# Kernel optimization log

Hardware: AMD Instinct MI355X
Metric: run time of the kernel (lower is better)

Reference implementation:

```python
import jax, jax.numpy as jnp
import numpy as np
from jax import lax

NPOINT = 1024
NSAMPLE = 32
RADIUS = 0.2
EPS = 1e-5  # BatchNorm eps (torch default)


def farthest_point_sample(xyz, npoint):
    # xyz: [B, N, 3] -> [B, npoint] int32 indices. Deterministic start at index 0
    # (torch version uses a random start; math is otherwise identical).
    B, N, _ = xyz.shape

    def step(carry, _):
        distance, farthest = carry
        centroid = jnp.take_along_axis(xyz, farthest[:, None, None], axis=1)  # [B,1,3]
        d = jnp.sum((xyz - centroid) ** 2, axis=-1)                            # [B,N]
        distance = jnp.minimum(distance, d)
        return (distance, jnp.argmax(distance, axis=-1).astype(jnp.int32)), farthest

    init = (jnp.full((B, N), 1e10, xyz.dtype), jnp.zeros((B,), jnp.int32))
    _, cents = lax.scan(step, init, None, length=npoint)  # [npoint, B]
    return cents.T


def query_ball_point(radius, nsample, xyz, new_xyz):
    # xyz: [B,N,3], new_xyz: [B,S,3] -> [B,S,nsample] int32 indices
    B, N, _ = xyz.shape
    S = new_xyz.shape[1]
    sqr = jnp.sum((new_xyz[:, :, None, :] - xyz[:, None, :, :]) ** 2, axis=-1)  # [B,S,N]
    base = jnp.broadcast_to(jnp.arange(N, dtype=jnp.int32), (B, S, N))
    idx = jnp.where(sqr > radius * radius, N, base)
    idx = jnp.sort(idx, axis=-1)[:, :, :nsample]
    first = idx[:, :, :1]
    return jnp.where(idx == N, first, idx)


def index_points(points, idx):
    # points: [B,N,C], idx: [B,...] -> [B,...,C]
    return jax.vmap(lambda p, i: p[i])(points, idx)


def conv_bn_relu(x, w, b, g, beta):
    # 1x1 Conv2d == per-point linear; BatchNorm2d in training mode (batch stats,
    # biased variance) over all dims except channel.
    y = jnp.einsum('bskc,oc->bsko', x, w) + b          # [B,S,K,O]
    m = jnp.mean(y, axis=(0, 1, 2), keepdims=True)
    v = jnp.var(y, axis=(0, 1, 2), keepdims=True)
    return jax.nn.relu((y - m) / jnp.sqrt(v + EPS) * g + beta)


def setup_inputs() -> dict:
    key = jax.random.key(0)
    ks = jax.random.split(key, 8)
    B, N, D = 16, 4096, 64
    xyz = jax.random.uniform(ks[0], (B, N, 3), dtype=jnp.float32)
    points = jax.random.normal(ks[1], (B, N, D), dtype=jnp.float32)
    chans = [D + 3, 64, 64, 128]
    inp = {'xyz': xyz, 'points': points}
    for i in range(3):
        cin, cout = chans[i], chans[i + 1]
        inp[f'w{i}'] = jax.random.normal(ks[2 + i], (cout, cin), dtype=jnp.float32) * (1.0 / np.sqrt(cin))
        inp[f'b{i}'] = jnp.zeros((cout,), jnp.float32)
        inp[f'g{i}'] = jnp.ones((cout,), jnp.float32)
        inp[f'be{i}'] = jnp.zeros((cout,), jnp.float32)
    return inp


def reference(xyz, points, w0, b0, g0, be0, w1, b1, g1, be1, w2, b2, g2, be2):
    fps_idx = farthest_point_sample(xyz, NPOINT)            # [B,S]
    new_xyz = index_points(xyz, fps_idx)                    # [B,S,3]
    group_idx = query_ball_point(RADIUS, NSAMPLE, xyz, new_xyz)  # [B,S,K]
    grouped_xyz = index_points(xyz, group_idx) - new_xyz[:, :, None, :]  # [B,S,K,3]
    feats = jnp.concatenate([grouped_xyz, index_points(points, group_idx)], axis=-1)
    for (w, b, g, be) in ((w0, b0, g0, be0), (w1, b1, g1, be1), (w2, b2, g2, be2)):
        feats = conv_bn_relu(feats, w, b, g, be)
    new_points = jnp.max(feats, axis=2)                     # max over nsample -> [B,S,C_out]
    return new_xyz, new_points
```

## Files before the change

kernel.cpp:

```cpp
#include <hip/hip_runtime.h>
#include <hip/hip_bf16.h>
#include <cstdint>
#include <cstddef>

#define NPTS   4096
#define NPT    1024
#define NSAMP  32
#define NBATCH 16
#define MROWS  (NBATCH*NPT*NSAMP)
#define NTILES (MROWS / 64)
#define EPSV   1e-5f

typedef __attribute__((ext_vector_type(8))) short bfrag;
typedef __attribute__((ext_vector_type(4))) float f32x4;

static __device__ __forceinline__ unsigned short f2bf(float f) {
  union { float f; unsigned u; } x; x.f = f;
  unsigned u = x.u;
  u += 0x7FFFu + ((u >> 16) & 1u);
  return (unsigned short)(u >> 16);
}
static __device__ __forceinline__ float bf2f(unsigned short h) {
  union { unsigned u; float f; } x; x.u = ((unsigned)h) << 16;
  return x.f;
}
static __device__ __forceinline__ unsigned cvt_pk_bf16(float lo, float hi) {
  unsigned r;
  asm("v_cvt_pk_bf16_f32 %0, %1, %2" : "=v"(r) : "v"(lo), "v"(hi));
  return r;
}

__global__ __launch_bounds__(256) void prep_kernel(
    const float* __restrict__ w0, const float* __restrict__ w1,
    const float* __restrict__ w2, unsigned short* __restrict__ wb0,
    unsigned short* __restrict__ wb1, unsigned short* __restrict__ wb2,
    int* __restrict__ flags) {
  const int tid = threadIdx.x;
  for (int i = tid; i < 260; i += 256) flags[i] = 0;
  for (int i = tid; i < 64 * 96; i += 256) {
    const int o = i / 96, c = i % 96;
    float v;
    if (c < 64)      v = w0[o * 67 + 3 + c];
    else if (c < 67) v = w0[o * 67 + (c - 64)];
    else             v = 0.f;
    wb0[i] = f2bf(v);
  }
  for (int i = tid; i < 64 * 64; i += 256) wb1[i] = f2bf(w1[i]);
  for (int i = tid; i < 128 * 64; i += 256) wb2[i] = f2bf(w2[i]);
}

#define FPS_T 256
#define PPT   (NPTS / FPS_T)
#define CHUNK 128

template <int CTRL>
static __device__ __forceinline__ float dpp_max_step(float v) {
  int t = __builtin_amdgcn_update_dpp(0, __float_as_int(v), CTRL, 0xF, 0xF, true);
  return fmaxf(v, __int_as_float(t));
}

__global__ __launch_bounds__(256) void k1_kernel(
    const float* __restrict__ xyz, const float* __restrict__ points,
    const unsigned short* __restrict__ Wb, float* __restrict__ newxyz,
    unsigned short* __restrict__ Y1, float* __restrict__ psum,
    float* __restrict__ psq, int* __restrict__ flags) {
  __shared__ __align__(16) float xs[NPTS];
  __shared__ __align__(16) float ys[NPTS];
  __shared__ __align__(16) float zs[NPTS];
  __shared__ __align__(16) float olds[NPT * 3];
  __shared__ __align__(16) uint2 sl[2][4];
  constexpr int KP = 104;
  __shared__ __align__(16) unsigned short As[64 * KP];
  __shared__ __align__(16) unsigned short ly[64 * 64];
  __shared__ float ssum[64], ssq[64];
  __shared__ int   gidxL[64];
  __shared__ float cents[8];
  __shared__ int   s_tile;

  const int tid = threadIdx.x;
  int* progress = flags;
  int* counter  = flags + 256;

  if (blockIdx.x < NBATCH) {
    const int b = blockIdx.x;
    const int wave = tid >> 6;
    const float* base = xyz + (size_t)b * NPTS * 3;
    float* outb = newxyz + (size_t)b * NPT * 3;
    int* prog = &progress[b * 16];
    for (int i = tid; i < NPTS; i += FPS_T) {
      xs[i] = base[3 * i + 0];
      ys[i] = base[3 * i + 1];
      zs[i] = base[3 * i + 2];
    }
    __syncthreads();

    const int p0 = tid * PPT;
    float px[PPT], py[PPT], pz[PPT], dist[PPT];
    #pragma unroll
    for (int i = 0; i < PPT; i += 4) {
      *(float4*)&px[i] = *(const float4*)&xs[p0 + i];
      *(float4*)&py[i] = *(const float4*)&ys[p0 + i];
      *(float4*)&pz[i] = *(const float4*)&zs[p0 + i];
    }
    #pragma unroll
    for (int i = 0; i < PPT; ++i) dist[i] = 1e10f;

    int cur = 0;
    for (int it = 0; it < NPT; ++it) {
      const float cx = xs[cur], cy = ys[cur], cz = zs[cur];
      if (tid == 0) {
        olds[3 * it + 0] = cx;
        olds[3 * it + 1] = cy;
        olds[3 * it + 2] = cz;
      }
      if ((it & (CHUNK - 1)) == CHUNK - 1) {
        __syncthreads();
        const int cs = it - (CHUNK - 1);
        if (tid < 96)
          *(float4*)&outb[cs * 3 + tid * 4] =
              *(const float4*)&olds[cs * 3 + tid * 4];
        __threadfence();
        __syncthreads();
        if (tid == 0) atomicAdd(prog, CHUNK);
      }
      if (it == NPT - 1) break;

      float bestv = -1.f; int besti = p0;
      #pragma unroll
      for (int i = 0; i < PPT; ++i) {
        const float dx = __fsub_rn(px[i], cx);
        const float dy = __fsub_rn(py[i], cy);
        const float dz = __fsub_rn(pz[i], cz);
        const float d = __fadd_rn(__fadd_rn(__fmul_rn(dx, dx), __fmul_rn(dy, dy)),
                                  __fmul_rn(dz, dz));
        const float nd = fminf(dist[i], d);
        dist[i] = nd;
        const bool g = nd > bestv;
        bestv = g ? nd : bestv;
        besti = g ? (p0 + i) : besti;
      }

      float m = bestv;
      m = dpp_max_step<0x111>(m);
      m = dpp_max_step<0x112>(m);
      m = dpp_max_step<0x114>(m);
      m = dpp_max_step<0x118>(m);
      m = dpp_max_step<0x142>(m);
      m = dpp_max_step<0x143>(m);
      const float wmax =
          __int_as_float(__builtin_amdgcn_readlane(__float_as_int(m), 63));

      const unsigned long long mask = __ballot(bestv == wmax);
      const int wl = __ffsll((long long)mask) - 1;
      const int widx = __builtin_amdgcn_readlane(besti, wl);

      const int buf = it & 1;
      if ((tid & 63) == 0)
        sl[buf][wave] = make_uint2(__float_as_uint(wmax), (unsigned)widx);
      __syncthreads();

      const uint4* p4 = (const uint4*)&sl[buf][0];
      const uint4 q0 = p4[0], q1 = p4[1];
      float bv; int bi;
      {
        bv = __uint_as_float(q0.x); bi = (int)q0.y;
        const float v1 = __uint_as_float(q0.z);
        if (v1 > bv) { bv = v1; bi = (int)q0.w; }
        const float v2 = __uint_as_float(q1.x);
        if (v2 > bv) { bv = v2; bi = (int)q1.y; }
        const float v3 = __uint_as_float(q1.z);
        if (v3 > bv) { bv = v3; bi = (int)q1.w; }
      }
      cur = bi;
    }
    return;
  }

  const int wave = tid >> 6, lane = tid & 63;
  for (;;) {
    if (tid == 0) {
      const int t0 = atomicAdd(counter, 1);
      s_tile = t0;
      if (t0 < NTILES) {
        const int b = t0 & 15, s0 = (t0 >> 4) * 2;
        while (__hip_atomic_load(&progress[b * 16], __ATOMIC_ACQUIRE,
                                 __HIP_MEMORY_SCOPE_AGENT) < s0 + 2)
          __builtin_amdgcn_s_sleep(2);
      }
    }
    __syncthreads();
    const int t = s_tile;
    if (t >= NTILES) break;
    const int b = t & 15, s0 = (t >> 4) * 2;

    if (wave < 2) {
      const int gs = b * NPT + s0 + wave;
      const float* base = xyz + (size_t)b * NPTS * 3;
      const float* c = newxyz + (size_t)gs * 3;
      const float cx = c[0], cy = c[1], cz = c[2];
      if (lane == 0) {
        cents[wave * 4 + 0] = cx;
        cents[wave * 4 + 1] = cy;
        cents[wave * 4 + 2] = cz;
      }
      const float R2 = (float)(0.2 * 0.2);
      int* g = &gidxL[wave * 32];
      int count = 0;
      int first = -1;
      for (int ch = 0; ch < NPTS / 64; ++ch) {
        const int i = ch * 64 + lane;
        const float dx = __fsub_rn(base[3 * i + 0], cx);
        const float dy = __fsub_rn(base[3 * i + 1], cy);
        const float dz = __fsub_rn(base[3 * i + 2], cz);
        const float d = __fadd_rn(
            __fadd_rn(__fmul_rn(dx, dx), __fmul_rn(dy, dy)), __fmul_rn(dz, dz));
        const bool pred = !(d > R2);
        const unsigned long long mask = __ballot(pred);
        if (mask) {
          if (count == 0) first = ch * 64 + (__ffsll((long long)mask) - 1);
          const int rank = __popcll(mask & ((1ull << lane) - 1ull));
          const int pos = count + rank;
          if (pred && pos < NSAMP) g[pos] = i;
          count += (int)__popcll(mask);
          if (count >= NSAMP) break;
        }
      }
      if (first < 0) first = 0;
      for (int j = count + lane; j < NSAMP; j += 64) g[j] = first;
    }
    if (tid < 64) { ssum[tid] = 0.f; ssq[tid] = 0.f; }
    __syncthreads();

    {
      const int row = tid >> 2, q = tid & 3;
      const int gpt = gidxL[row];
      const float* pf = points + ((size_t)b * NPTS + gpt) * 64 + 16 * q;
      float f[16];
      #pragma unroll
      for (int i = 0; i < 4; ++i)
        *(float4*)&f[4 * i] = *(const float4*)&pf[4 * i];
      uint4 u0, u1;
      u0.x = cvt_pk_bf16(f[0], f[1]);   u0.y = cvt_pk_bf16(f[2], f[3]);
      u0.z = cvt_pk_bf16(f[4], f[5]);   u0.w = cvt_pk_bf16(f[6], f[7]);
      u1.x = cvt_pk_bf16(f[8], f[9]);   u1.y = cvt_pk_bf16(f[10], f[11]);
      u1.z = cvt_pk_bf16(f[12], f[13]); u1.w = cvt_pk_bf16(f[14], f[15]);
      uint4* dst = (uint4*)&As[row * KP + 16 * q];
      dst[0] = u0; dst[1] = u1;
      if (q == 0) {
        const float* px = xyz + ((size_t)b * NPTS + gpt) * 3;
        const float* pc = &cents[(row >> 5) * 4];
        const float rx = px[0] - pc[0];
        const float ry = px[1] - pc[1];
        const float rz = px[2] - pc[2];
        uint4* d2 = (uint4*)&As[row * KP + 64];
        d2[0] = uint4{cvt_pk_bf16(rx, ry), cvt_pk_bf16(rz, 0.f), 0u, 0u};
        d2[1] = uint4{0u, 0u, 0u, 0u};
        d2[2] = uint4{0u, 0u, 0u, 0u};
        d2[3] = uint4{0u, 0u, 0u, 0u};
      }
    }
    __syncthreads();

    const int l15 = lane & 15, kq = lane >> 4;
    const unsigned short* abase = &As[(wave * 16 + l15) * KP + kq * 8];
    const bfrag a0 = *(const bfrag*)abase;
    const bfrag a1 = *(const bfrag*)(abase + 32);
    const bfrag a2 = *(const bfrag*)(abase + 64);

    #pragma unroll
    for (int nt = 0; nt < 4; ++nt) {
      const unsigned short* wsrc = Wb + (size_t)(nt * 16 + l15) * 96 + kq * 8;
      const bfrag b0 = *(const bfrag*)wsrc;
      const bfrag b1 = *(const bfrag*)(wsrc + 32);
      const bfrag b2 = *(const bfrag*)(wsrc + 64);
      f32x4 acc = {0.f, 0.f, 0.f, 0.f};
      acc = __builtin_amdgcn_mfma_f32_16x16x32_bf16(a0, b0, acc, 0, 0, 0);
      acc = __builtin_amdgcn_mfma_f32_16x16x32_bf16(a1, b1, acc, 0, 0, 0);
      acc = __builtin_amdgcn_mfma_f32_16x16x32_bf16(a2, b2, acc, 0, 0, 0);

      float s = acc[0] + acc[1] + acc[2] + acc[3];
      float q = acc[0]*acc[0] + acc[1]*acc[1] + acc[2]*acc[2] + acc[3]*acc[3];
      s += __shfl_xor(s, 16); q += __shfl_xor(q, 16);
      s += __shfl_xor(s, 32); q += __shfl_xor(q, 32);
      if (kq == 0) {
        atomicAdd(&ssum[nt * 16 + l15], s);
        atomicAdd(&ssq [nt * 16 + l15], q);
      }
      const unsigned p01 = cvt_pk_bf16(acc[0], acc[1]);
      const unsigned p23 = cvt_pk_bf16(acc[2], acc[3]);
      const int colo = nt * 16 + l15;
      const int rbase = wave * 16 + kq * 4;
      ly[(rbase + 0) * 64 + colo] = (unsigned short)(p01 & 0xffffu);
      ly[(rbase + 1) * 64 + colo] = (unsigned short)(p01 >> 16);
      ly[(rbase + 2) * 64 + colo] = (unsigned short)(p23 & 0xffffu);
      ly[(rbase + 3) * 64 + colo] = (unsigned short)(p23 >> 16);
    }
    __syncthreads();
    {
      const size_t r0 = (size_t)b * 32768 + (size_t)(t >> 4) * 64;
      const uint4* lsrc = (const uint4*)ly;
      uint4* gdst = (uint4*)(Y1 + r0 * 64);
      #pragma unroll
      for (int i = tid; i < 64 * 64 * 2 / 16; i += 256) gdst[i] = lsrc[i];
    }
    if (tid < 64) {
      psum[(size_t)t * 64 + tid] = ssum[tid];
      psq [(size_t)t * 64 + tid] = ssq [tid];
    }
    __syncthreads();
  }
}

static __device__ __forceinline__ bfrag affine_relu_frag(
    const unsigned short* __restrict__ src, const float* __restrict__ st,
    int c0) {
  union { bfrag f; unsigned u[4]; } r;
  const uint4 raw = *(const uint4*)src;
  const unsigned w[4] = {raw.x, raw.y, raw.z, raw.w};
  #pragma unroll
  for (int p = 0; p < 4; ++p) {
    const int c = c0 + 2 * p;
    float lo = bf2f((unsigned short)(w[p] & 0xffffu));
    float hi = bf2f((unsigned short)(w[p] >> 16));
    lo = fmaxf(fmaf(lo, st[2 * c + 0], st[2 * c + 1]), 0.f);
    hi = fmaxf(fmaf(hi, st[2 * c + 2], st[2 * c + 3]), 0.f);
    r.u[p] = cvt_pk_bf16(lo, hi);
  }
  return r.f;
}

template <int COUT, int WAVES>
__global__ __launch_bounds__(WAVES * 64) void mm_mfma_kernel(
    const unsigned short* __restrict__ Xin, const unsigned short* __restrict__ Wb,
    const float* __restrict__ stin, unsigned short* __restrict__ Y,
    float* __restrict__ psum, float* __restrict__ psq) {
  constexpr int NT = COUT / 16;
  constexpr int ROWS = WAVES * 16;
  __shared__ float ssum[COUT], ssq[COUT];
  __shared__ __align__(16) unsigned short ly[ROWS * COUT];
  const int tid = threadIdx.x, bid = blockIdx.x;
  const int wave = tid >> 6, lane = tid & 63;
  const int l15 = lane & 15, kq = lane >> 4;
  const size_t r0 = (size_t)bid * ROWS;
  if (tid < COUT) { ssum[tid] = 0.f; ssq[tid] = 0.f; }

  const int arow = wave * 16 + l15;
  const unsigned short* asrc = Xin + (r0 + arow) * 64 + kq * 8;
  const bfrag a0 = affine_relu_frag(asrc, stin, kq * 8);
  const bfrag a1 = affine_relu_frag(asrc + 32, stin, 32 + kq * 8);
  __syncthreads();

  #pragma unroll
  for (int nt = 0; nt < NT; ++nt) {
    const unsigned short* wsrc = Wb + (size_t)(nt * 16 + l15) * 64 + kq * 8;
    const bfrag b0 = *(const bfrag*)wsrc;
    const bfrag b1 = *(const bfrag*)(wsrc + 32);
    f32x4 acc = {0.f, 0.f, 0.f, 0.f};
    acc = __builtin_amdgcn_mfma_f32_16x16x32_bf16(a0, b0, acc, 0, 0, 0);
    acc = __builtin_amdgcn_mfma_f32_16x16x32_bf16(a1, b1, acc, 0, 0, 0);

    float s = acc[0] + acc[1] + acc[2] + acc[3];
    float q = acc[0]*acc[0] + acc[1]*acc[1] + acc[2]*acc[2] + acc[3]*acc[3];
    s += __shfl_xor(s, 16); q += __shfl_xor(q, 16);
    s += __shfl_xor(s, 32); q += __shfl_xor(q, 32);
    if (kq == 0) {
      atomicAdd(&ssum[nt * 16 + l15], s);
      atomicAdd(&ssq [nt * 16 + l15], q);
    }
    const unsigned p01 = cvt_pk_bf16(acc[0], acc[1]);
    const unsigned p23 = cvt_pk_bf16(acc[2], acc[3]);
    const int colo = nt * 16 + l15;
    const int rbase = wave * 16 + kq * 4;
    ly[(rbase + 0) * COUT + colo] = (unsigned short)(p01 & 0xffffu);
    ly[(rbase + 1) * COUT + colo] = (unsigned short)(p01 >> 16);
    ly[(rbase + 2) * COUT + colo] = (unsigned short)(p23 & 0xffffu);
    ly[(rbase + 3) * COUT + colo] = (unsigned short)(p23 >> 16);
  }
  __syncthreads();
  {
    const uint4* lsrc = (const uint4*)ly;
    uint4* gdst = (uint4*)(Y + r0 * COUT);
    #pragma unroll
    for (int i = tid; i < ROWS * COUT * 2 / 16; i += WAVES * 64) gdst[i] = lsrc[i];
  }
  if (tid < COUT) {
    psum[(size_t)bid * COUT + tid] = ssum[tid];
    psq [(size_t)bid * COUT + tid] = ssq [tid];
  }
}

__global__ __launch_bounds__(512) void mm3_pool_kernel(
    const unsigned short* __restrict__ Xin, const unsigned short* __restrict__ Wb,
    const float* __restrict__ stin, float* __restrict__ pooled,
    float* __restrict__ psum, float* __restrict__ psq) {
  constexpr int COUT = 128, NT = 8;
  __shared__ float ssum[COUT], ssq[COUT];
  __shared__ float pm[8][COUT];
  const int tid = threadIdx.x, bid = blockIdx.x;
  const int wave = tid >> 6, lane = tid & 63;
  const int l15 = lane & 15, kq = lane >> 4;
  const size_t r0 = (size_t)bid * 128;
  if (tid < COUT) { ssum[tid] = 0.f; ssq[tid] = 0.f; }

  const int arow = wave * 16 + l15;
  const unsigned short* asrc = Xin + (r0 + arow) * 64 + kq * 8;
  const bfrag a0 = affine_relu_frag(asrc, stin, kq * 8);
  const bfrag a1 = affine_relu_frag(asrc + 32, stin, 32 + kq * 8);
  __syncthreads();

  #pragma unroll
  for (int nt = 0; nt < NT; ++nt) {
    const unsigned short* wsrc = Wb + (size_t)(nt * 16 + l15) * 64 + kq * 8;
    const bfrag b0 = *(const bfrag*)wsrc;
    const bfrag b1 = *(const bfrag*)(wsrc + 32);
    f32x4 acc = {0.f, 0.f, 0.f, 0.f};
    acc = __builtin_amdgcn_mfma_f32_16x16x32_bf16(a0, b0, acc, 0, 0, 0);
    acc = __builtin_amdgcn_mfma_f32_16x16x32_bf16(a1, b1, acc, 0, 0, 0);

    float s = acc[0] + acc[1] + acc[2] + acc[3];
    float q = acc[0]*acc[0] + acc[1]*acc[1] + acc[2]*acc[2] + acc[3]*acc[3];
    s += __shfl_xor(s, 16); q += __shfl_xor(q, 16);
    s += __shfl_xor(s, 32); q += __shfl_xor(q, 32);
    float mx = fmaxf(fmaxf(acc[0], acc[1]), fmaxf(acc[2], acc[3]));
    mx = fmaxf(mx, __shfl_xor(mx, 16));
    mx = fmaxf(mx, __shfl_xor(mx, 32));
    if (kq == 0) {
      atomicAdd(&ssum[nt * 16 + l15], s);
      atomicAdd(&ssq [nt * 16 + l15], q);
      pm[wave][nt * 16 + l15] = mx;
    }
  }
  __syncthreads();
  {
    const int g = tid >> 7, col = tid & 127;
    const float v = fmaxf(pm[2 * g][col], pm[2 * g + 1][col]);
    pooled[(r0 >> 5) * COUT + g * COUT + col] = v;
  }
  if (tid < COUT) {
    psum[(size_t)bid * COUT + tid] = ssum[tid];
    psq [(size_t)bid * COUT + tid] = ssq [tid];
  }
}

__global__ __launch_bounds__(256) void finalize_kernel(
    const float* __restrict__ psum, const float* __restrict__ psq,
    const float* __restrict__ gam, const float* __restrict__ bet,
    float* __restrict__ st, int C, int nb) {
  const int c = blockIdx.x, tid = threadIdx.x;
  float s = 0.f, q = 0.f;
  for (int i = tid; i < nb; i += 256) {
    s += psum[(size_t)i * C + c];
    q += psq [(size_t)i * C + c];
  }
  #pragma unroll
  for (int off = 32; off > 0; off >>= 1) {
    s += __shfl_down(s, off);
    q += __shfl_down(q, off);
  }
  __shared__ float as_[4], aq_[4];
  if ((tid & 63) == 0) { as_[tid >> 6] = s; aq_[tid >> 6] = q; }
  __syncthreads();
  if (tid == 0) {
    s = as_[0] + as_[1] + as_[2] + as_[3];
    q = aq_[0] + aq_[1] + aq_[2] + aq_[3];
    const float invM = 1.f / (float)MROWS;
    const float mean = s * invM;
    const float var = q * invM - mean * mean;
    const float inv = 1.f / sqrtf(var + EPSV);
    const float sc = gam[c] * inv;
    st[2 * c + 0] = sc;
    st[2 * c + 1] = bet[c] - mean * sc;
  }
}

__global__ __launch_bounds__(256) void bn_relu_kernel(
    const float* __restrict__ pooled, const float* __restrict__ st,
    float* __restrict__ out) {
  __shared__ float s_st[256];
  const int tid = threadIdx.x;
  s_st[tid] = st[tid];
  __syncthreads();
  const int n4 = NBATCH * NPT * 128 / 4;
  for (int i = blockIdx.x * 256 + tid; i < n4; i += gridDim.x * 256) {
    float4 v = ((const float4*)pooled)[i];
    const int c0 = (i * 4) & 127;
    v.x = fmaxf(fmaf(v.x, s_st[2 * c0 + 0], s_st[2 * c0 + 1]), 0.f);
    v.y = fmaxf(fmaf(v.y, s_st[2 * c0 + 2], s_st[2 * c0 + 3]), 0.f);
    v.z = fmaxf(fmaf(v.z, s_st[2 * c0 + 4], s_st[2 * c0 + 5]), 0.f);
    v.w = fmaxf(fmaf(v.w, s_st[2 * c0 + 6], s_st[2 * c0 + 7]), 0.f);
    ((float4*)out)[i] = v;
  }
}

extern "C" void kernel_launch(void* const* d_in, const int* in_sizes, int n_in,
                              void* d_out, int out_size, void* d_ws, size_t ws_size,
                              hipStream_t stream) {
  (void)in_sizes; (void)n_in; (void)out_size; (void)ws_size;
  const float* xyz    = (const float*)d_in[0];
  const float* points = (const float*)d_in[1];
  const float* w0 = (const float*)d_in[2];
  const float* g0 = (const float*)d_in[4];
  const float* be0 = (const float*)d_in[5];
  const float* w1 = (const float*)d_in[6];
  const float* g1 = (const float*)d_in[8];
  const float* be1 = (const float*)d_in[9];
  const float* w2 = (const float*)d_in[10];
  const float* g2 = (const float*)d_in[12];
  const float* be2 = (const float*)d_in[13];

  float* out = (float*)d_out;
  float* newxyz = out;
  float* newpts = out + (size_t)NBATCH * NPT * 3;

  char* ws = (char*)d_ws;
  unsigned short* Y1 = (unsigned short*)ws;
  float* P3 = (float*)ws;
  unsigned short* Y2 = (unsigned short*)(ws + 134217728);
  int*   flags = (int*)(ws + 201326592);
  float* psum = (float*)(ws + 203423744);
  float* psq  = (float*)(ws + 205520896);
  float* st   = (float*)(ws + 207618048);
  float* st1 = st, *st2 = st + 256, *st3 = st + 512;
  unsigned short* wb0 = (unsigned short*)(ws + 207621120);
  unsigned short* wb1 = (unsigned short*)(ws + 207621120 + 12288);
  unsigned short* wb2 = (unsigned short*)(ws + 207621120 + 12288 + 8192);

  prep_kernel<<<1, 256, 0, stream>>>(w0, w1, w2, wb0, wb1, wb2, flags);
  k1_kernel<<<256, 256, 0, stream>>>(xyz, points, wb0, newxyz, Y1, psum, psq, flags);
  finalize_kernel<<<64, 256, 0, stream>>>(psum, psq, g0, be0, st1, 64, NTILES);
  mm_mfma_kernel<64, 4><<<MROWS / 64, 256, 0, stream>>>(Y1, wb1, st1, Y2, psum, psq);
  finalize_kernel<<<64, 256, 0, stream>>>(psum, psq, g1, be1, st2, 64, MROWS / 64);
  mm3_pool_kernel<<<MROWS / 128, 512, 0, stream>>>(Y2, wb2, st2, P3, psum, psq);
  finalize_kernel<<<128, 256, 0, stream>>>(psum, psq, g2, be2, st3, 128, MROWS / 128);
  bn_relu_kernel<<<2048, 256, 0, stream>>>(P3, st3, newpts);
}
```

Measured before the change: 902.1 us.

## Process four centroids per tile in fused FPS/grouping kernel, smaller FPS chunks

The consumer blocks of the fused kernel now handle 4 centroids (128 rows) per tile instead of 2, with all four waves running the ball query and each wave computing two 16-row MFMA sub-tiles. This reuses the B fragments across two row blocks and halves the number of tile handoffs and stat-partial writes. The FPS publish chunk is reduced from 128 to 64 so consumers can start sooner. The cost is more LDS per block and one extra flush/sync cycle per chunk in the FPS producers.

```diff
diff --git a/kernel.cpp b/kernel.cpp
--- a/kernel.cpp
+++ b/kernel.cpp
@@ -8,7 +8,7 @@
 #define NSAMP  32
 #define NBATCH 16
 #define MROWS  (NBATCH*NPT*NSAMP)
-#define NTILES (MROWS / 64)
+#define NTILES4 (MROWS / 128)
 #define EPSV   1e-5f
 
 typedef __attribute__((ext_vector_type(8))) short bfrag;
@@ -51,7 +51,7 @@
 
 #define FPS_T 256
 #define PPT   (NPTS / FPS_T)
-#define CHUNK 128
+#define CHUNK 64
 
 template <int CTRL>
 static __device__ __forceinline__ float dpp_max_step(float v) {
@@ -70,11 +70,11 @@
   __shared__ __align__(16) float olds[NPT * 3];
   __shared__ __align__(16) uint2 sl[2][4];
   constexpr int KP = 104;
-  __shared__ __align__(16) unsigned short As[64 * KP];
-  __shared__ __align__(16) unsigned short ly[64 * 64];
+  __shared__ __align__(16) unsigned short As[128 * KP];
+  __shared__ __align__(16) unsigned short ly[128 * 64];
   __shared__ float ssum[64], ssq[64];
-  __shared__ int   gidxL[64];
-  __shared__ float cents[8];
+  __shared__ int   gidxL[128];
+  __shared__ float cents[16];
   __shared__ int   s_tile;
 
   const int tid = threadIdx.x;
@@ -116,7 +116,7 @@
       if ((it & (CHUNK - 1)) == CHUNK - 1) {
         __syncthreads();
         const int cs = it - (CHUNK - 1);
-        if (tid < 96)
+        if (tid < CHUNK * 3 / 4)
           *(float4*)&outb[cs * 3 + tid * 4] =
               *(const float4*)&olds[cs * 3 + tid * 4];
         __threadfence();
@@ -181,19 +181,19 @@
     if (tid == 0) {
       const int t0 = atomicAdd(counter, 1);
       s_tile = t0;
-      if (t0 < NTILES) {
-        const int b = t0 & 15, s0 = (t0 >> 4) * 2;
+      if (t0 < NTILES4) {
+        const int b = t0 & 15, s0 = (t0 >> 4) * 4;
         while (__hip_atomic_load(&progress[b * 16], __ATOMIC_ACQUIRE,
-                                 __HIP_MEMORY_SCOPE_AGENT) < s0 + 2)
+                                 __HIP_MEMORY_SCOPE_AGENT) < s0 + 4)
           __builtin_amdgcn_s_sleep(2);
       }
     }
     __syncthreads();
     const int t = s_tile;
-    if (t >= NTILES) break;
-    const int b = t & 15, s0 = (t >> 4) * 2;
-
-    if (wave < 2) {
+    if (t >= NTILES4) break;
+    const int b = t & 15, s0 = (t >> 4) * 4;
+
+    {
       const int gs = b * NPT + s0 + wave;
       const float* base = xyz + (size_t)b * NPTS * 3;
       const float* c = newxyz + (size_t)gs * 3;
@@ -232,20 +232,23 @@
     __syncthreads();
 
     {
-      const int row = tid >> 2, q = tid & 3;
+      const int row = tid >> 1, q = tid & 1;
       const int gpt = gidxL[row];
-      const float* pf = points + ((size_t)b * NPTS + gpt) * 64 + 16 * q;
-      float f[16];
+      const float* pf = points + ((size_t)b * NPTS + gpt) * 64 + 32 * q;
+      float f[32];
       #pragma unroll
-      for (int i = 0; i < 4; ++i)
+      for (int i = 0; i < 8; ++i)
         *(float4*)&f[4 * i] = *(const float4*)&pf[4 * i];
-      uint4 u0, u1;
-      u0.x = cvt_pk_bf16(f[0], f[1]);   u0.y = cvt_pk_bf16(f[2], f[3]);
-      u0.z = cvt_pk_bf16(f[4], f[5]);   u0.w = cvt_pk_bf16(f[6], f[7]);
-      u1.x = cvt_pk_bf16(f[8], f[9]);   u1.y = cvt_pk_bf16(f[10], f[11]);
-      u1.z = cvt_pk_bf16(f[12], f[13]); u1.w = cvt_pk_bf16(f[14], f[15]);
-      uint4* dst = (uint4*)&As[row * KP + 16 * q];
-      dst[0] = u0; dst[1] = u1;
+      uint4* dst = (uint4*)&As[row * KP + 32 * q];
+      #pragma unroll
+      for (int v = 0; v < 4; ++v) {
+        uint4 u;
+        u.x = cvt_pk_bf16(f[8 * v + 0], f[8 * v + 1]);
+        u.y = cvt_pk_bf16(f[8 * v + 2], f[8 * v + 3]);
+        u.z = cvt_pk_bf16(f[8 * v + 4], f[8 * v + 5]);
+        u.w = cvt_pk_bf16(f[8 * v + 6], f[8 * v + 7]);
+        dst[v] = u;
+      }
       if (q == 0) {
         const float* px = xyz + ((size_t)b * NPTS + gpt) * 3;
         const float* pc = &cents[(row >> 5) * 4];
@@ -262,10 +265,15 @@
     __syncthreads();
 
     const int l15 = lane & 15, kq = lane >> 4;
-    const unsigned short* abase = &As[(wave * 16 + l15) * KP + kq * 8];
-    const bfrag a0 = *(const bfrag*)abase;
-    const bfrag a1 = *(const bfrag*)(abase + 32);
-    const bfrag a2 = *(const bfrag*)(abase + 64);
+    bfrag a0[2], a1[2], a2[2];
+    #pragma unroll
+    for (int p = 0; p < 2; ++p) {
+      const unsigned short* abase =
+          &As[(wave * 32 + p * 16 + l15) * KP + kq * 8];
+      a0[p] = *(const bfrag*)abase;
+      a1[p] = *(const bfrag*)(abase + 32);
+      a2[p] = *(const bfrag*)(abase + 64);
+    }
 
     #pragma unroll
     for (int nt = 0; nt < 4; ++nt) {
@@ -273,35 +281,38 @@
       const bfrag b0 = *(const bfrag*)wsrc;
       const bfrag b1 = *(const bfrag*)(wsrc + 32);
       const bfrag b2 = *(const bfrag*)(wsrc + 64);
-      f32x4 acc = {0.f, 0.f, 0.f, 0.f};
-      acc = __builtin_amdgcn_mfma_f32_16x16x32_bf16(a0, b0, acc, 0, 0, 0);
-      acc = __builtin_amdgcn_mfma_f32_16x16x32_bf16(a1, b1, acc, 0, 0, 0);
-      acc = __builtin_amdgcn_mfma_f32_16x16x32_bf16(a2, b2, acc, 0, 0, 0);
-
-      float s = acc[0] + acc[1] + acc[2] + acc[3];
-      float q = acc[0]*acc[0] + acc[1]*acc[1] + acc[2]*acc[2] + acc[3]*acc[3];
-      s += __shfl_xor(s, 16); q += __shfl_xor(q, 16);
-      s += __shfl_xor(s, 32); q += __shfl_xor(q, 32);
+      float sT = 0.f, qT = 0.f;
+      #pragma unroll
+      for (int p = 0; p < 2; ++p) {
+        f32x4 acc = {0.f, 0.f, 0.f, 0.f};
+        acc = __builtin_amdgcn_mfma_f32_16x16x32_bf16(a0[p], b0, acc, 0, 0, 0);
+        acc = __builtin_amdgcn_mfma_f32_16x16x32_bf16(a1[p], b1, acc, 0, 0, 0);
+        acc = __builtin_amdgcn_mfma_f32_16x16x32_bf16(a2[p], b2, acc, 0, 0, 0);
+        sT += acc[0] + acc[1] + acc[2] + acc[3];
+        qT += acc[0]*acc[0] + acc[1]*acc[1] + acc[2]*acc[2] + acc[3]*acc[3];
+        const unsigned p01 = cvt_pk_bf16(acc[0], acc[1]);
+        const unsigned p23 = cvt_pk_bf16(acc[2], acc[3]);
+        const int colo = nt * 16 + l15;
+        const int rbase = wave * 32 + p * 16 + kq * 4;
+        ly[(rbase + 0) * 64 + colo] = (unsigned short)(p01 & 0xffffu);
+        ly[(rbase + 1) * 64 + colo] = (unsigned short)(p01 >> 16);
+        ly[(rbase + 2) * 64 + colo] = (unsigned short)(p23 & 0xffffu);
+        ly[(rbase + 3) * 64 + colo] = (unsigned short)(p23 >> 16);
+      }
+      sT += __shfl_xor(sT, 16); qT += __shfl_xor(qT, 16);
+      sT += __shfl_xor(sT, 32); qT += __shfl_xor(qT, 32);
       if (kq == 0) {
-        atomicAdd(&ssum[nt * 16 + l15], s);
-        atomicAdd(&ssq [nt * 16 + l15], q);
-      }
-      const unsigned p01 = cvt_pk_bf16(acc[0], acc[1]);
-      const unsigned p23 = cvt_pk_bf16(acc[2], acc[3]);
-      const int colo = nt * 16 + l15;
-      const int rbase = wave * 16 + kq * 4;
-      ly[(rbase + 0) * 64 + colo] = (unsigned short)(p01 & 0xffffu);
-      ly[(rbase + 1) * 64 + colo] = (unsigned short)(p01 >> 16);
-      ly[(rbase + 2) * 64 + colo] = (unsigned short)(p23 & 0xffffu);
-      ly[(rbase + 3) * 64 + colo] = (unsigned short)(p23 >> 16);
+        atomicAdd(&ssum[nt * 16 + l15], sT);
+        atomicAdd(&ssq [nt * 16 + l15], qT);
+      }
     }
     __syncthreads();
     {
-      const size_t r0 = (size_t)b * 32768 + (size_t)(t >> 4) * 64;
+      const size_t r0 = ((size_t)b * NPT + s0) * 32;
       const uint4* lsrc = (const uint4*)ly;
       uint4* gdst = (uint4*)(Y1 + r0 * 64);
       #pragma unroll
-      for (int i = tid; i < 64 * 64 * 2 / 16; i += 256) gdst[i] = lsrc[i];
+      for (int i = tid; i < 128 * 64 * 2 / 16; i += 256) gdst[i] = lsrc[i];
     }
     if (tid < 64) {
       psum[(size_t)t * 64 + tid] = ssum[tid];
@@ -527,7 +538,7 @@
 
   prep_kernel<<<1, 256, 0, stream>>>(w0, w1, w2, wb0, wb1, wb2, flags);
   k1_kernel<<<256, 256, 0, stream>>>(xyz, points, wb0, newxyz, Y1, psum, psq, flags);
-  finalize_kernel<<<64, 256, 0, stream>>>(psum, psq, g0, be0, st1, 64, NTILES);
+  finalize_kernel<<<64, 256, 0, stream>>>(psum, psq, g0, be0, st1, 64, NTILES4);
   mm_mfma_kernel<64, 4><<<MROWS / 64, 256, 0, stream>>>(Y1, wb1, st1, Y2, psum, psq);
   finalize_kernel<<<64, 256, 0, stream>>>(psum, psq, g1, be1, st2, 64, MROWS / 64);
   mm3_pool_kernel<<<MROWS / 128, 512, 0, stream>>>(Y2, wb2, st2, P3, psum, psq);
```

New measurement: 919.1 us. About the same (+1.9%).
